# Optimization experiments

Hardware: AMD Instinct MI355X
Metric: run time of the kernel (lower is better)

The kernel has to match this reference:

```python
import jax, jax.numpy as jnp
import numpy as np

H, C = 2, 32  # heads, out_channels per head
NEG_SLOPE = 0.2


def gatv2_layer(h, src, dst, ea, W, b, We, att, bias, N):
    # shared lin_l = lin_r (share_weights=True)
    z = (h @ W + b).reshape(N, H, C)                      # [N,H,C]
    e = (ea @ We).reshape(-1, H, C)                        # [E',H,C]
    s = jax.nn.leaky_relu(z[dst] + z[src] + e, NEG_SLOPE)  # [E',H,C]
    alpha = jnp.einsum('ehc,hc->eh', s, att)               # [E',H]
    # segment softmax over destination neighborhoods
    m = jax.ops.segment_max(alpha, dst, num_segments=N)
    m = jnp.where(jnp.isfinite(m), m, 0.0)
    ex = jnp.exp(alpha - m[dst])
    denom = jax.ops.segment_sum(ex, dst, num_segments=N)
    a = ex / (denom[dst] + 1e-16)                          # [E',H]
    msg = (z[src] * a[:, :, None]).reshape(-1, H * C)      # [E',H*C]
    out = jax.ops.segment_sum(msg, dst, num_segments=N) + bias
    return out                                             # [N,H*C]


def setup_inputs() -> dict:
    key = jax.random.key(0)
    ks = jax.random.split(key, 16)
    N, E = 50000, 800000
    inp = {
        'x': jax.random.normal(ks[0], (N, 2), jnp.float32),
        'edge_index': jax.random.randint(ks[1], (2, E), 0, N, jnp.int64 if jax.config.jax_enable_x64 else jnp.int32).astype(jnp.int32),
        'edge_attr': jax.random.uniform(ks[2], (E, 2), jnp.float32),
        'dest_index': 123,
        'W0': jax.random.normal(ks[3], (2, 64), jnp.float32) * 0.5,
        'b0': jnp.zeros((64,), jnp.float32),
        'We0': jax.random.normal(ks[4], (2, 64), jnp.float32) * 0.5,
        'att0': jax.random.normal(ks[5], (H, C), jnp.float32) * 0.5,
        'bias0': jnp.zeros((64,), jnp.float32),
        'W1': jax.random.normal(ks[6], (64, 64), jnp.float32) * 0.125,
        'b1': jnp.zeros((64,), jnp.float32),
        'We1': jax.random.normal(ks[7], (2, 64), jnp.float32) * 0.5,
        'att1': jax.random.normal(ks[8], (H, C), jnp.float32) * 0.5,
        'bias1': jnp.zeros((64,), jnp.float32),
        'Wm1': jax.random.normal(ks[9], (194, 32), jnp.float32) * 0.07,
        'bm1': jnp.zeros((32,), jnp.float32),
        'Wm2': jax.random.normal(ks[10], (32, 1), jnp.float32) * 0.17,
        'bm2': jnp.zeros((1,), jnp.float32),
    }
    return inp


def reference(x, edge_index, edge_attr, dest_index,
              W0, b0, We0, att0, bias0,
              W1, b1, We1, att1, bias1,
              Wm1, bm1, Wm2, bm2):
    N = x.shape[0]
    # add self loops (fill_value='mean' for edge_attr)
    loops = jnp.arange(N, dtype=edge_index.dtype)
    src = jnp.concatenate([edge_index[0], loops])
    dst = jnp.concatenate([edge_index[1], loops])
    ea_sl = jnp.concatenate(
        [edge_attr, jnp.broadcast_to(edge_attr.mean(axis=0), (N, edge_attr.shape[1]))], axis=0)

    h = x
    h = jax.nn.elu(gatv2_layer(h, src, dst, ea_sl, W0, b0, We0, att0, bias0, N))
    h = jax.nn.elu(gatv2_layer(h, src, dst, ea_sl, W1, b1, We1, att1, bias1, N))

    goal = h[dest_index]                                   # [64]
    src_emb = h[edge_index[0]]                             # [E,64]
    dst_emb = h[edge_index[1]]                             # [E,64]
    goal_rep = jnp.broadcast_to(goal, (edge_index.shape[1], goal.shape[0]))
    edge_in = jnp.concatenate([src_emb, dst_emb, goal_rep, edge_attr], axis=-1)  # [E,194]
    hmlp = jax.nn.relu(edge_in @ Wm1 + bm1)
    logits = (hmlp @ Wm2 + bm2).squeeze(-1)                # [E]
    return logits
```

## Files before the change

### kernel.cpp

```cpp
#include <hip/hip_runtime.h>
#include <hip/hip_bf16.h>
#include <hip/hip_fp16.h>
#include <math.h>


typedef __attribute__((ext_vector_type(8))) short short8;
typedef __attribute__((ext_vector_type(4))) float f32x4;

#define BSH 5
#define CAP 1024
#define CH 4096

template <int IMM>
__device__ __forceinline__ float swz(float x) {
    return __int_as_float(__builtin_amdgcn_ds_swizzle(__float_as_int(x), IMM));
}

template <int CTRL>
__device__ __forceinline__ float dpp_add(float p) {
    int t = __builtin_amdgcn_update_dpp(0, __float_as_int(p), CTRL, 0xF, 0xF, true);
    return p + __int_as_float(t);
}

__device__ __forceinline__ short2 bsplit(float x) {
    unsigned u = __float_as_uint(x);
    short hi = (short)(u >> 16);
    float hif = __uint_as_float(u & 0xFFFF0000u);
    short lo = (short)(__float_as_uint(x - hif) >> 16);
    return make_short2(hi, lo);
}

__global__ __launch_bounds__(512) void setup_kernel(const float* __restrict__ W1,
                                                    const float* __restrict__ Wm1,
                                                    short* __restrict__ BfW1,
                                                    short* __restrict__ BfWm,
                                                    int* __restrict__ bucket_cursor,
                                                    float* __restrict__ easum, int nbuck) {
    if (blockIdx.x == 2) {
        for (int i = threadIdx.x; i < nbuck; i += 512) bucket_cursor[i] = i * CAP;
        if (threadIdx.x < 2) easum[threadIdx.x] = 0.f;
        return;
    }
    int snt = threadIdx.x >> 6;
    int lane = threadIdx.x & 63;
    int s = snt >> 2, nt = snt & 3;
    int col = nt * 16 + (lane & 15);
    short* Bf = blockIdx.x == 0 ? BfW1 : BfWm;
#pragma unroll
    for (int j = 0; j < 8; ++j) {
        int k = s * 32 + (lane >> 4) * 8 + j;
        float v;
        if (blockIdx.x == 0) {
            v = W1[k * 64 + col];
        } else {
            v = (col < 32) ? Wm1[k * 32 + col] : Wm1[(64 + k) * 32 + (col - 32)];
        }
        short2 t = bsplit(v);
        Bf[(snt * 2 + 0) * 512 + lane * 8 + j] = t.x;
        Bf[(snt * 2 + 1) * 512 + lane * 8 + j] = t.y;
    }
}

__global__ __launch_bounds__(256) void phaseA_kernel(const int* __restrict__ ei,
                                                     const float2* __restrict__ ea,
                                                     int* __restrict__ bucket_cursor,
                                                     float* __restrict__ easum,
                                                     float4* __restrict__ staged,
                                                     int E, int nbuck) {
    extern __shared__ int sm[];
    int* lcnt = sm;
    int* lbase = sm + nbuck;
    __shared__ float r0[4], r1[4];
    int tid = threadIdx.x;
    for (int i = tid; i < nbuck; i += 256) lcnt[i] = 0;
    __syncthreads();
    int base = blockIdx.x * CH;
    int end = min(base + CH, E);
    for (int i = base + tid; i < end; i += 256) {
        int d = ei[E + i];
        atomicAdd(&lcnt[d >> BSH], 1);
    }
    __syncthreads();
    for (int i = tid; i < nbuck; i += 256) {
        int c = lcnt[i];
        lbase[i] = c ? atomicAdd(&bucket_cursor[i], c) : 0;
        lcnt[i] = 0;
    }
    __syncthreads();
    float s0 = 0.f, s1 = 0.f;
    for (int i = base + tid; i < end; i += 256) {
        int s = ei[i], d = ei[E + i];
        float2 v = ea[i];
        s0 += v.x; s1 += v.y;
        int b = d >> BSH;
        int pos = lbase[b] + atomicAdd(&lcnt[b], 1);
        staged[pos] = make_float4(__int_as_float(s), v.x, v.y, __int_as_float(d));
    }
#pragma unroll
    for (int o = 32; o >= 1; o >>= 1) {
        s0 += __shfl_xor(s0, o);
        s1 += __shfl_xor(s1, o);
    }
    int wave = tid >> 6;
    if ((tid & 63) == 0) { r0[wave] = s0; r1[wave] = s1; }
    __syncthreads();
    if (tid == 0) {
        atomicAdd(&easum[0], r0[0] + r0[1] + r0[2] + r0[3]);
        atomicAdd(&easum[1], r1[0] + r1[1] + r1[2] + r1[3]);
    }
}

__global__ __launch_bounds__(512, 8) void phaseB_mega(
    const float4* __restrict__ staged, const int* __restrict__ bucket_cursor,
    const float* __restrict__ easum, const float2* __restrict__ x,
    const float* __restrict__ W0, const float* __restrict__ b0,
    const float* __restrict__ We, const float* __restrict__ att,
    const float* __restrict__ bias, const short* __restrict__ Bf,
    const float* __restrict__ b1,
    int* __restrict__ row_ptr, float4* __restrict__ recs,
    __half* __restrict__ z16, int N, int E, int nbuck) {
    __shared__ int cnt32[32];
    __shared__ int offs[32];
    __shared__ int psum8[8];
    __shared__ float acc7[32][7];
    __shared__ float h0s[32 * 64];
    int b = blockIdx.x;
    int n0g = b << BSH;
    int tid = threadIdx.x;
    int lane = tid & 63;
    int wave = tid >> 6;
    int local = 0;
    for (int j = tid; j < b; j += 512) local += bucket_cursor[j] - j * CAP;
#pragma unroll
    for (int o = 32; o >= 1; o >>= 1) local += __shfl_xor(local, o);
    if (tid < 32) cnt32[tid] = 0;
    for (int i = tid; i < 32 * 7; i += 512) ((float*)acc7)[i] = 0.f;
    if (lane == 0) psum8[wave] = local;
    __syncthreads();
    int bbase = 32 * b + psum8[0] + psum8[1] + psum8[2] + psum8[3]
                       + psum8[4] + psum8[5] + psum8[6] + psum8[7];
    int sbeg = b * CAP;
    int send = bucket_cursor[b];
    int nsl = send - sbeg;
    int nodes_here = min(32, N - n0g);
    int nrec = nsl + nodes_here;
    float invE = 1.f / (float)E;
    float m0 = easum[0] * invE, m1 = easum[1] * invE;

    {
        int sub = lane & 15;
        int eslot = lane >> 4;
        int ch0 = ((sub & 7) << 2) + ((sub >> 3) << 5);
        float Wx[4], Wy[4], bc[4], w0e[4], w1e[4], at[4];
#pragma unroll
        for (int j = 0; j < 4; ++j) {
            Wx[j] = W0[ch0 + j];  Wy[j] = W0[64 + ch0 + j];  bc[j] = b0[ch0 + j];
            w0e[j] = We[ch0 + j]; w1e[j] = We[64 + ch0 + j]; at[j] = att[ch0 + j];
        }
        int npass = (nsl + 3) >> 2;
        for (int p = wave; p < npass; p += 8) {
            int idx = p * 4 + eslot;
            bool valid = idx < nsl;
            float4 r = staged[sbeg + (valid ? idx : nsl - 1)];
            int s = __float_as_int(r.x);
            int d = __float_as_int(r.w);
            float2 xs = x[s];
            float2 xd = x[d];
            float P = 0.f;
#pragma unroll
            for (int j = 0; j < 4; ++j) {
                float zs = fmaf(xs.x, Wx[j], fmaf(xs.y, Wy[j], bc[j]));
                float zd = fmaf(xd.x, Wx[j], fmaf(xd.y, Wy[j], bc[j]));
                float t0 = zd + zs + fmaf(r.y, w0e[j], r.z * w1e[j]);
                t0 = fmaxf(t0, 0.2f * t0);
                P = fmaf(t0, at[j], P);
            }
            P += swz<0x041F>(P);
            P += swz<0x081F>(P);
            P += swz<0x101F>(P);
            float Po = swz<0x201F>(P);
            float Ph0 = (sub < 8) ? P : Po;
            float Ph1 = (sub < 8) ? Po : P;
            float w0 = __expf(fminf(Ph0, 60.f));
            float w1 = __expf(fminf(Ph1, 60.f));
            if (sub == 0 && valid) {
                int dl = d - n0g;
                atomicAdd(&acc7[dl][0], w0);
                atomicAdd(&acc7[dl][1], w0 * xs.x);
                atomicAdd(&acc7[dl][2], w0 * xs.y);
                atomicAdd(&acc7[dl][3], w1);
                atomicAdd(&acc7[dl][4], w1 * xs.x);
                atomicAdd(&acc7[dl][5], w1 * xs.y);
                atomicAdd(&cnt32[dl], 1);
            }
        }
    }
    __syncthreads();

    if (wave == 0) {
        int node = n0g + lane;
        bool ok = (lane < 32) && (node < N);
        int tot = (lane < 32) ? (cnt32[lane] + ((node < N) ? 1 : 0)) : 0;
        int v = tot;
#pragma unroll
        for (int st = 1; st < 32; st <<= 1) {
            int u = __shfl_up(v, st);
            if (lane >= st) v += u;
        }
        if (ok) {
            int excl = bbase + v - tot;
            row_ptr[node] = excl;
            recs[excl] = make_float4(__int_as_float(node), m0, m1, __int_as_float(node));
            offs[lane] = excl + 1;
        }
        if (b == nbuck - 1 && lane == 0) row_ptr[N] = bbase + nrec;
    }
    for (int k = 0; k < 4; ++k) {
        int q = wave + 8 * k;
        int ch = lane;
        int node = n0g + q;
        float hv = 0.f;
        if (node < N) {
            float2 xn = x[node];
            float W0c = W0[ch], W0c2 = W0[64 + ch], b0c = b0[ch];
            float zn = fmaf(xn.x, W0c, fmaf(xn.y, W0c2, b0c));
            float ts = fmaf(2.f, zn, fmaf(m0, We[ch], m1 * We[64 + ch]));
            ts = fmaxf(ts, 0.2f * ts);
            float p = ts * att[ch];
#pragma unroll
            for (int o = 1; o <= 16; o <<= 1) p += __shfl_xor(p, o);
            float wself = __expf(fminf(p, 60.f));
            int hsel = (ch >= 32) ? 3 : 0;
            float l  = acc7[q][hsel]     + wself;
            float Sx = acc7[q][hsel + 1] + wself * xn.x;
            float Sy = acc7[q][hsel + 2] + wself * xn.y;
            float num = fmaf(W0c, Sx, fmaf(W0c2, Sy, b0c * l));
            float v = num / (l + 1e-16f) + bias[ch];
            hv = (v > 0.f) ? v : expm1f(v);
        }
        h0s[q * 64 + ch] = hv;
    }
    __syncthreads();

    int m = lane & 15, quad = lane >> 4;
    int rowb = (wave & 1) * 16 + m;
    int nt = wave >> 1;
    f32x4 acc = {0.f, 0.f, 0.f, 0.f};
#pragma unroll
    for (int s = 0; s < 2; ++s) {
        const float* ap = h0s + rowb * 64 + s * 32 + quad * 8;
        float4 a0 = *(const float4*)ap;
        float4 a1 = *(const float4*)(ap + 4);
        short8 ahi, alo;
        short2 t;
        t = bsplit(a0.x); ahi[0] = t.x; alo[0] = t.y;
        t = bsplit(a0.y); ahi[1] = t.x; alo[1] = t.y;
        t = bsplit(a0.z); ahi[2] = t.x; alo[2] = t.y;
        t = bsplit(a0.w); ahi[3] = t.x; alo[3] = t.y;
        t = bsplit(a1.x); ahi[4] = t.x; alo[4] = t.y;
        t = bsplit(a1.y); ahi[5] = t.x; alo[5] = t.y;
        t = bsplit(a1.z); ahi[6] = t.x; alo[6] = t.y;
        t = bsplit(a1.w); ahi[7] = t.x; alo[7] = t.y;
        const short* bp = Bf + ((s * 4 + nt) * 2) * 512 + lane * 8;
        short8 bhi = *(const short8*)bp;
        short8 blo = *(const short8*)(bp + 512);
        acc = __builtin_amdgcn_mfma_f32_16x16x32_bf16(ahi, bhi, acc, 0, 0, 0);
        acc = __builtin_amdgcn_mfma_f32_16x16x32_bf16(ahi, blo, acc, 0, 0, 0);
        acc = __builtin_amdgcn_mfma_f32_16x16x32_bf16(alo, bhi, acc, 0, 0, 0);
    }
    {
        int col = nt * 16 + m;
        float bj = b1[col];
#pragma unroll
        for (int r = 0; r < 4; ++r) {
            int orow = n0g + (wave & 1) * 16 + quad * 4 + r;
            if (orow < N) z16[(size_t)orow * 64 + col] = __float2half(acc[r] + bj);
        }
    }
    for (int i = sbeg + tid; i < send; i += 512) {
        float4 r = staged[i];
        int d = __float_as_int(r.w);
        int pos = atomicAdd(&offs[d - n0g], 1);
        recs[pos] = r;
    }
}

__global__ __launch_bounds__(256) void agg1_kernel(
    const __half* __restrict__ z, const int* __restrict__ row_ptr,
    const float4* __restrict__ recs,
    const float* __restrict__ We, const float* __restrict__ att,
    const float* __restrict__ bias, float* __restrict__ hout, int N) {
    int gtid = blockIdx.x * blockDim.x + threadIdx.x;
    int n = gtid >> 6;
    if (n >= N) return;
    n = __builtin_amdgcn_readfirstlane(n);
    int lane = threadIdx.x & 63;
    int half = lane >> 5;
    int c = (lane & 31) * 2;

    float We0a = We[c],      We0b = We[c + 1];
    float We1a = We[64 + c], We1b = We[64 + c + 1];
    float atta = att[c],     attb = att[c + 1];
    float2 znf = __half22float2(*(const __half2*)(z + (size_t)n * 64 + c));

    int beg = row_ptr[n], end = row_ptr[n + 1];
    float ll[4] = {0.f, 0.f, 0.f, 0.f};
    float a0[4] = {0.f, 0.f, 0.f, 0.f};
    float a1[4] = {0.f, 0.f, 0.f, 0.f};
    for (int i = beg; i < end; i += 8) {
        float w[4]; float2 zs[4];
#pragma unroll
        for (int k = 0; k < 4; ++k) {
            int idx = i + 2 * k + half;
            int idc = idx < end ? idx : end - 1;
            float4 r = recs[idc];
            int s = __float_as_int(r.x);
            zs[k] = __half22float2(*(const __half2*)(z + (size_t)s * 64 + c));
            float sj0 = znf.x + zs[k].x + fmaf(r.y, We0a, r.z * We1a);
            float sj1 = znf.y + zs[k].y + fmaf(r.y, We0b, r.z * We1b);
            sj0 = fmaxf(sj0, 0.2f * sj0);
            sj1 = fmaxf(sj1, 0.2f * sj1);
            float p = fmaf(sj0, atta, sj1 * attb);
            p = dpp_add<0xB1>(p);
            p = dpp_add<0x4E>(p);
            p = dpp_add<0x141>(p);
            p = dpp_add<0x140>(p);
            float ww = __expf(fminf(p, 60.f));
            w[k] = (idx < end) ? ww : 0.f;
        }
#pragma unroll
        for (int k = 0; k < 4; ++k) {
            ll[k] += w[k];
            a0[k] = fmaf(w[k], zs[k].x, a0[k]);
            a1[k] = fmaf(w[k], zs[k].y, a1[k]);
        }
    }
    float l  = (ll[0] + ll[1]) + (ll[2] + ll[3]);
    float s0 = (a0[0] + a0[1]) + (a0[2] + a0[3]);
    float s1 = (a1[0] + a1[1]) + (a1[2] + a1[3]);
    l  += __shfl_xor(l, 32);
    s0 += __shfl_xor(s0, 32);
    s1 += __shfl_xor(s1, 32);
    float inv = 1.f / (l + 1e-16f);
    float v0 = s0 * inv + bias[c];
    float v1 = s1 * inv + bias[c + 1];
    v0 = (v0 > 0.f) ? v0 : expm1f(v0);
    v1 = (v1 > 0.f) ? v1 : expm1f(v1);
    *(float2*)(hout + (size_t)n * 64 + c) = make_float2(v0, v1);
}

__global__ __launch_bounds__(256) void mfma_gemm64(const float* __restrict__ h,
                                                   const short* __restrict__ Bf,
                                                   __half* __restrict__ out, int N,
                                                   const float* __restrict__ Wm1,
                                                   const float* __restrict__ bm1,
                                                   const int* __restrict__ dest,
                                                   float* __restrict__ gv) {
    int wave = threadIdx.x >> 6;
    int lane = threadIdx.x & 63;
    int n0 = blockIdx.x * 64 + wave * 16;
    if (n0 < N) {
        int m = lane & 15, quad = lane >> 4;
        int arow = n0 + m;
        if (arow > N - 1) arow = N - 1;
        f32x4 acc[4] = {{0.f, 0.f, 0.f, 0.f}, {0.f, 0.f, 0.f, 0.f},
                        {0.f, 0.f, 0.f, 0.f}, {0.f, 0.f, 0.f, 0.f}};
#pragma unroll
        for (int s = 0; s < 2; ++s) {
            const float* ap = h + (size_t)arow * 64 + s * 32 + quad * 8;
            float4 a0 = *(const float4*)ap;
            float4 a1 = *(const float4*)(ap + 4);
            short8 ahi, alo;
            short2 t;
            t = bsplit(a0.x); ahi[0] = t.x; alo[0] = t.y;
            t = bsplit(a0.y); ahi[1] = t.x; alo[1] = t.y;
            t = bsplit(a0.z); ahi[2] = t.x; alo[2] = t.y;
            t = bsplit(a0.w); ahi[3] = t.x; alo[3] = t.y;
            t = bsplit(a1.x); ahi[4] = t.x; alo[4] = t.y;
            t = bsplit(a1.y); ahi[5] = t.x; alo[5] = t.y;
            t = bsplit(a1.z); ahi[6] = t.x; alo[6] = t.y;
            t = bsplit(a1.w); ahi[7] = t.x; alo[7] = t.y;
#pragma unroll
            for (int nt = 0; nt < 4; ++nt) {
                const short* bp = Bf + ((s * 4 + nt) * 2) * 512 + lane * 8;
                short8 bhi = *(const short8*)bp;
                short8 blo = *(const short8*)(bp + 512);
                acc[nt] = __builtin_amdgcn_mfma_f32_16x16x32_bf16(ahi, bhi, acc[nt], 0, 0, 0);
                acc[nt] = __builtin_amdgcn_mfma_f32_16x16x32_bf16(ahi, blo, acc[nt], 0, 0, 0);
                acc[nt] = __builtin_amdgcn_mfma_f32_16x16x32_bf16(alo, bhi, acc[nt], 0, 0, 0);
            }
        }
#pragma unroll
        for (int nt = 0; nt < 4; ++nt) {
            int col = nt * 16 + m;
#pragma unroll
            for (int r = 0; r < 4; ++r) {
                int orow = n0 + quad * 4 + r;
                if (orow < N) out[(size_t)orow * 64 + col] = __float2half(acc[nt][r]);
            }
        }
    }
    if (gv && blockIdx.x == 0 && threadIdx.x < 32) {
        int dd = dest[0];
        int q = threadIdx.x;
        float acc2 = bm1[q];
        for (int k = 0; k < 64; ++k)
            acc2 = fmaf(h[(size_t)dd * 64 + k], Wm1[(128 + k) * 32 + q], acc2);
        gv[q] = acc2;
    }
}

__global__ __launch_bounds__(256) void edge_mlp_kernel(
    const int* __restrict__ ei, const float2* __restrict__ ea,
    const __half* __restrict__ hsd, const float* __restrict__ gvec,
    const float* __restrict__ WrowA, const float* __restrict__ WrowB,
    const float* __restrict__ Wm2, const float* __restrict__ bm2,
    float* __restrict__ out, int E) {
    int tid = blockIdx.x * blockDim.x + threadIdx.x;
    int e = tid >> 3;
    int j = tid & 7;
    if (e >= E) return;
    int s = ei[e], d = ei[E + e];
    float2 eav = ea[e];
    const __half2* ps = (const __half2*)(hsd + (size_t)s * 64 + j * 4);
    const __half2* pd = (const __half2*)(hsd + (size_t)d * 64 + 32 + j * 4);
    float2 a01 = __half22float2(ps[0]), a23 = __half22float2(ps[1]);
    float2 b01 = __half22float2(pd[0]), b23 = __half22float2(pd[1]);
    float4 g = *(const float4*)(gvec + j * 4);
    float4 wa = *(const float4*)(WrowA + j * 4);
    float4 wb = *(const float4*)(WrowB + j * 4);
    float4 w2 = *(const float4*)(Wm2 + j * 4);
    float acc = 0.f, v;
    v = fmaf(eav.x, wa.x, fmaf(eav.y, wb.x, a01.x + b01.x + g.x)); v = fmaxf(v, 0.f); acc = fmaf(v, w2.x, acc);
    v = fmaf(eav.x, wa.y, fmaf(eav.y, wb.y, a01.y + b01.y + g.y)); v = fmaxf(v, 0.f); acc = fmaf(v, w2.y, acc);
    v = fmaf(eav.x, wa.z, fmaf(eav.y, wb.z, a23.x + b23.x + g.z)); v = fmaxf(v, 0.f); acc = fmaf(v, w2.z, acc);
    v = fmaf(eav.x, wa.w, fmaf(eav.y, wb.w, a23.y + b23.y + g.w)); v = fmaxf(v, 0.f); acc = fmaf(v, w2.w, acc);
    acc = dpp_add<0xB1>(acc);
    acc = dpp_add<0x4E>(acc);
    acc = dpp_add<0x141>(acc);
    if (j == 0) out[e] = acc + bm2[0];
}

extern "C" void kernel_launch(void* const* d_in, const int* in_sizes, int n_in,
                              void* d_out, int out_size, void* d_ws, size_t ws_size,
                              hipStream_t stream) {
    const float* x     = (const float*)d_in[0];
    const int*   ei    = (const int*)d_in[1];
    const float* ea    = (const float*)d_in[2];
    const int*   dest  = (const int*)d_in[3];
    const float* W0    = (const float*)d_in[4];
    const float* b0    = (const float*)d_in[5];
    const float* We0   = (const float*)d_in[6];
    const float* att0  = (const float*)d_in[7];
    const float* bias0 = (const float*)d_in[8];
    const float* W1    = (const float*)d_in[9];
    const float* b1    = (const float*)d_in[10];
    const float* We1   = (const float*)d_in[11];
    const float* att1  = (const float*)d_in[12];
    const float* bias1 = (const float*)d_in[13];
    const float* Wm1   = (const float*)d_in[14];
    const float* bm1   = (const float*)d_in[15];
    const float* Wm2   = (const float*)d_in[16];
    const float* bm2   = (const float*)d_in[17];

    const int N = in_sizes[0] / 2;
    const int E = in_sizes[1] / 2;
    const int nbuck = (N + 31) >> BSH;
    const int nchunk = (E + CH - 1) / CH;

    char* ws = (char*)d_ws;
    size_t off = 0;
    auto alloc = [&](size_t bytes) -> void* {
        void* p = ws + off;
        off += bytes;
        off = (off + 255) & ~(size_t)255;
        return p;
    };
    int*    bucket_cursor = (int*)alloc((size_t)nbuck * 4);
    int*    row_ptr       = (int*)alloc((size_t)(N + 1) * 4);
    size_t  slack_bytes   = (size_t)nbuck * CAP * 16;
    float4* staged        = (float4*)alloc(slack_bytes);
    float4* recs          = (float4*)alloc((size_t)(E + N) * 16);
    __half* z16           = (__half*)alloc((size_t)N * 64 * 2);
    float*  hbuf          = (float*)alloc((size_t)N * 64 * 4);
    float*  easum         = (float*)alloc(8);
    float*  gvec          = (float*)alloc(32 * 4);
    short*  BfW1          = (short*)alloc(8192 * 2);
    short*  BfWm          = (short*)alloc(8192 * 2);
    __half* hsd16         = z16;

    dim3 blk(256);
    setup_kernel<<<3, 512, 0, stream>>>(W1, Wm1, BfW1, BfWm, bucket_cursor, easum, nbuck);
    phaseA_kernel<<<nchunk, blk, (size_t)nbuck * 8, stream>>>(ei, (const float2*)ea,
                                                              bucket_cursor, easum,
                                                              staged, E, nbuck);
    phaseB_mega<<<nbuck, 512, 0, stream>>>(staged, bucket_cursor, easum,
                                           (const float2*)x, W0, b0, We0, att0, bias0,
                                           BfW1, b1, row_ptr, recs, z16, N, E, nbuck);
    agg1_kernel<<<(N * 64 + 255) / 256, blk, 0, stream>>>(z16, row_ptr, recs,
                                                          We1, att1, bias1, hbuf, N);
    mfma_gemm64<<<(N + 63) / 64, blk, 0, stream>>>(hbuf, BfWm, hsd16, N,
                                                   Wm1, bm1, dest, gvec);
    edge_mlp_kernel<<<((size_t)E * 8 + 255) / 256, blk, 0, stream>>>(
        ei, (const float2*)ea, hsd16, gvec,
        Wm1 + 192 * 32, Wm1 + 193 * 32, Wm2, bm2, (float*)d_out, E);
}
```

Before: 251.4 us.

## Bucket edges with direct global atomics and fold layer-0 projection algebra

The edge bucketing kernel drops its per-chunk shared-memory histogram (count, reserve, then scatter) and instead does one global atomicAdd on the bucket cursor per edge, in a grid-stride loop over 1024 blocks. This removes a second pass over the destination indices, two block barriers and a large dynamic shared allocation per block, but puts up to 800K atomics on global memory spread over about 1.5K bucket counters. Separately, the layer-0 score computation adds the source and destination features before multiplying by the weights and uses a doubled bias, which saves a few FMAs per channel.

```diff
diff --git a/kernel.cpp b/kernel.cpp
--- a/kernel.cpp
+++ b/kernel.cpp
@@ -9,7 +9,6 @@
 
 #define BSH 5
 #define CAP 1024
-#define CH 4096
 
 template <int IMM>
 __device__ __forceinline__ float swz(float x) {
@@ -66,34 +65,17 @@
                                                      int* __restrict__ bucket_cursor,
                                                      float* __restrict__ easum,
                                                      float4* __restrict__ staged,
-                                                     int E, int nbuck) {
-    extern __shared__ int sm[];
-    int* lcnt = sm;
-    int* lbase = sm + nbuck;
+                                                     int E) {
     __shared__ float r0[4], r1[4];
     int tid = threadIdx.x;
-    for (int i = tid; i < nbuck; i += 256) lcnt[i] = 0;
-    __syncthreads();
-    int base = blockIdx.x * CH;
-    int end = min(base + CH, E);
-    for (int i = base + tid; i < end; i += 256) {
-        int d = ei[E + i];
-        atomicAdd(&lcnt[d >> BSH], 1);
-    }
-    __syncthreads();
-    for (int i = tid; i < nbuck; i += 256) {
-        int c = lcnt[i];
-        lbase[i] = c ? atomicAdd(&bucket_cursor[i], c) : 0;
-        lcnt[i] = 0;
-    }
-    __syncthreads();
+    int gid = blockIdx.x * 256 + tid;
+    int stride = gridDim.x * 256;
     float s0 = 0.f, s1 = 0.f;
-    for (int i = base + tid; i < end; i += 256) {
+    for (int i = gid; i < E; i += stride) {
         int s = ei[i], d = ei[E + i];
         float2 v = ea[i];
         s0 += v.x; s1 += v.y;
-        int b = d >> BSH;
-        int pos = lbase[b] + atomicAdd(&lcnt[b], 1);
+        int pos = atomicAdd(&bucket_cursor[d >> BSH], 1);
         staged[pos] = make_float4(__int_as_float(s), v.x, v.y, __int_as_float(d));
     }
 #pragma unroll
@@ -151,10 +133,10 @@
         int sub = lane & 15;
         int eslot = lane >> 4;
         int ch0 = ((sub & 7) << 2) + ((sub >> 3) << 5);
-        float Wx[4], Wy[4], bc[4], w0e[4], w1e[4], at[4];
+        float Wx[4], Wy[4], bc2[4], w0e[4], w1e[4], at[4];
 #pragma unroll
         for (int j = 0; j < 4; ++j) {
-            Wx[j] = W0[ch0 + j];  Wy[j] = W0[64 + ch0 + j];  bc[j] = b0[ch0 + j];
+            Wx[j] = W0[ch0 + j];  Wy[j] = W0[64 + ch0 + j];  bc2[j] = 2.f * b0[ch0 + j];
             w0e[j] = We[ch0 + j]; w1e[j] = We[64 + ch0 + j]; at[j] = att[ch0 + j];
         }
         int npass = (nsl + 3) >> 2;
@@ -166,12 +148,12 @@
             int d = __float_as_int(r.w);
             float2 xs = x[s];
             float2 xd = x[d];
+            float sx = xs.x + xd.x, sy = xs.y + xd.y;
             float P = 0.f;
 #pragma unroll
             for (int j = 0; j < 4; ++j) {
-                float zs = fmaf(xs.x, Wx[j], fmaf(xs.y, Wy[j], bc[j]));
-                float zd = fmaf(xd.x, Wx[j], fmaf(xd.y, Wy[j], bc[j]));
-                float t0 = zd + zs + fmaf(r.y, w0e[j], r.z * w1e[j]);
+                float t0 = fmaf(sx, Wx[j], fmaf(sy, Wy[j],
+                            fmaf(r.y, w0e[j], fmaf(r.z, w1e[j], bc2[j]))));
                 t0 = fmaxf(t0, 0.2f * t0);
                 P = fmaf(t0, at[j], P);
             }
@@ -466,7 +448,6 @@
     const int N = in_sizes[0] / 2;
     const int E = in_sizes[1] / 2;
     const int nbuck = (N + 31) >> BSH;
-    const int nchunk = (E + CH - 1) / CH;
 
     char* ws = (char*)d_ws;
     size_t off = 0;
@@ -491,9 +472,8 @@
 
     dim3 blk(256);
     setup_kernel<<<3, 512, 0, stream>>>(W1, Wm1, BfW1, BfWm, bucket_cursor, easum, nbuck);
-    phaseA_kernel<<<nchunk, blk, (size_t)nbuck * 8, stream>>>(ei, (const float2*)ea,
-                                                              bucket_cursor, easum,
-                                                              staged, E, nbuck);
+    phaseA_kernel<<<1024, blk, 0, stream>>>(ei, (const float2*)ea,
+                                            bucket_cursor, easum, staged, E);
     phaseB_mega<<<nbuck, 512, 0, stream>>>(staged, bucket_cursor, easum,
                                            (const float2*)x, W0, b0, We0, att0, bias0,
                                            BfW1, b1, row_ptr, recs, z16, N, E, nbuck);
```

After: 360.2 us. 1.43x slower.
